# Kernel optimization log

Measured on AMD Instinct MI355X. Metric: run time of the kernel, lower is better.

Reference implementation:

```python
import jax, jax.numpy as jnp
import numpy as np

B, N, E, H = 8, 2048, 768, 8
D = E // H  # head dim = 96


def setup_inputs() -> dict:
    key = jax.random.key(0)
    ks = jax.random.split(key, 9)
    s = 0.02
    return {
        "x": jax.random.normal(ks[0], (B, N, E), dtype=jnp.float32),
        "Wq": jax.random.normal(ks[1], (E, E), dtype=jnp.float32) * s,
        "bq": jax.random.normal(ks[2], (E,), dtype=jnp.float32) * s,
        "Wk": jax.random.normal(ks[3], (E, E), dtype=jnp.float32) * s,
        "bk": jax.random.normal(ks[4], (E,), dtype=jnp.float32) * s,
        "Wv": jax.random.normal(ks[5], (E, E), dtype=jnp.float32) * s,
        "bv": jax.random.normal(ks[6], (E,), dtype=jnp.float32) * s,
        "Wo": jax.random.normal(ks[7], (E, E), dtype=jnp.float32) * s,
        "bo": jax.random.normal(ks[8], (E,), dtype=jnp.float32) * s,
    }


def _split_heads(t):
    # [b, n, (h d)] -> [b, h, n, d]
    b, n, e = t.shape
    return t.reshape(b, n, H, D).transpose(0, 2, 1, 3)


def reference(x, Wq, bq, Wk, bk, Wv, bv, Wo, bo):
    q = _split_heads(x @ Wq + bq)
    k = _split_heads(x @ Wk + bk)
    v = _split_heads(x @ Wv + bv)
    energy = jnp.einsum("bhqd,bhkd->bhqk", q, k)
    # Faithful quirk of the source: softmax first, THEN divide by sqrt(emb_size)
    att = jax.nn.softmax(energy, axis=-1) / jnp.sqrt(jnp.float32(E))
    out = jnp.einsum("bhqk,bhkd->bhqd", att, v)
    out = out.transpose(0, 2, 1, 3).reshape(x.shape[0], x.shape[1], E)
    return out @ Wo + bo
```

## Files before the change

### kernel.cpp

```cpp
#include <hip/hip_runtime.h>
#include <hip/hip_bf16.h>
#include <stdint.h>

#define BATCH 8
#define NSEQ  2048
#define EMB   768
#define NH    8
#define HD    96

typedef unsigned short u16;
typedef __attribute__((ext_vector_type(8))) short short8;
typedef __attribute__((ext_vector_type(4))) float f32x4;
typedef __attribute__((ext_vector_type(16))) float f32x16;

static __device__ __forceinline__ u16 f2bf(float f) {
  union { float f; uint32_t u; } c{f};
  uint32_t u = c.u;
  return (u16)((u + 0x7FFFu + ((u >> 16) & 1u)) >> 16);
}

__global__ __launch_bounds__(256) void k_convert_x(const float* __restrict__ x,
                                                   u16* __restrict__ xb) {
  size_t i = ((size_t)blockIdx.x * 256 + threadIdx.x) * 8;
  float4 a = *(const float4*)(x + i);
  float4 b = *(const float4*)(x + i + 4);
  short8 o;
  o[0] = f2bf(a.x); o[1] = f2bf(a.y); o[2] = f2bf(a.z); o[3] = f2bf(a.w);
  o[4] = f2bf(b.x); o[5] = f2bf(b.y); o[6] = f2bf(b.z); o[7] = f2bf(b.w);
  *(short8*)(xb + i) = o;
}

__global__ __launch_bounds__(256) void k_wtrans(const float* __restrict__ Wq,
                                                const float* __restrict__ Wk,
                                                const float* __restrict__ Wv,
                                                const float* __restrict__ Wo,
                                                u16* __restrict__ WTall) {
  int z = blockIdx.z;
  const float* W = (z == 0) ? Wq : (z == 1) ? Wk : (z == 2) ? Wv : Wo;
  u16* WT = WTall + (size_t)z * EMB * EMB;
  __shared__ float tile[32][33];
  int o0 = blockIdx.x * 32, i0 = blockIdx.y * 32;
  int tx = threadIdx.x, ty = threadIdx.y;
#pragma unroll
  for (int r = 0; r < 4; ++r)
    tile[ty * 4 + r][tx] = W[(size_t)(i0 + ty * 4 + r) * EMB + o0 + tx];
  __syncthreads();
#pragma unroll
  for (int r = 0; r < 4; ++r)
    WT[(size_t)(o0 + ty * 4 + r) * EMB + i0 + tx] = f2bf(tile[tx][ty * 4 + r]);
}

template <bool OUTF32>
static __device__ __forceinline__ void gemm_body(const u16* __restrict__ A,
                                                 const u16* __restrict__ WT,
                                                 const float* __restrict__ bias,
                                                 void* __restrict__ out,
                                                 int m0, int n0, float oscale) {
  __shared__ u16 As[128 * 64];
  __shared__ u16 Bs[128 * 64];
  const int t = threadIdx.x;
  const int w = t >> 6, l = t & 63;
  const int lr = l & 15, lg = l >> 4;
  const int wm = (w >> 1) * 64, wn = (w & 1) * 64;
  f32x4 acc[4][4] = {};
  for (int kt = 0; kt < 12; ++kt) {
    const int k0 = kt * 64;
#pragma unroll
    for (int i = 0; i < 4; ++i) {
      int g = (w * 4 + i) * 64 + l;
      int m = g >> 3, k8 = (g & 7) * 8;
      const u16* sa = A + (size_t)(m0 + m) * EMB + k0 + k8;
      __builtin_amdgcn_global_load_lds((const __attribute__((address_space(1))) void*)sa,
                                       (__attribute__((address_space(3))) void*)&As[(w * 4 + i) * 512],
                                       16, 0, 0);
      const u16* sb = WT + (size_t)(n0 + m) * EMB + k0 + k8;
      __builtin_amdgcn_global_load_lds((const __attribute__((address_space(1))) void*)sb,
                                       (__attribute__((address_space(3))) void*)&Bs[(w * 4 + i) * 512],
                                       16, 0, 0);
    }
    __syncthreads();
#pragma unroll
    for (int ks = 0; ks < 2; ++ks) {
      short8 af[4], bfr[4];
#pragma unroll
      for (int mf = 0; mf < 4; ++mf)
        af[mf] = *(const short8*)&As[(wm + mf * 16 + lr) * 64 + ks * 32 + lg * 8];
#pragma unroll
      for (int nf = 0; nf < 4; ++nf)
        bfr[nf] = *(const short8*)&Bs[(wn + nf * 16 + lr) * 64 + ks * 32 + lg * 8];
#pragma unroll
      for (int mf = 0; mf < 4; ++mf)
#pragma unroll
        for (int nf = 0; nf < 4; ++nf)
          acc[mf][nf] = __builtin_amdgcn_mfma_f32_16x16x32_bf16(af[mf], bfr[nf], acc[mf][nf], 0, 0, 0);
    }
    __syncthreads();
  }
#pragma unroll
  for (int nf = 0; nf < 4; ++nf) {
    int col = n0 + wn + nf * 16 + lr;
    float bv = bias[col];
#pragma unroll
    for (int mf = 0; mf < 4; ++mf)
#pragma unroll
      for (int r = 0; r < 4; ++r) {
        int row = m0 + wm + mf * 16 + lg * 4 + r;
        float v = (acc[mf][nf][r] + bv) * oscale;
        if (OUTF32)
          ((float*)out)[(size_t)row * EMB + col] = v;
        else
          ((u16*)out)[(size_t)row * EMB + col] = f2bf(v);
      }
  }
}

__global__ __launch_bounds__(256) void k_qkv_gemm(const u16* __restrict__ X,
                                                  const u16* __restrict__ WTall,
                                                  const float* __restrict__ bq,
                                                  const float* __restrict__ bk,
                                                  const float* __restrict__ bv,
                                                  u16* __restrict__ Q, u16* __restrict__ K,
                                                  u16* __restrict__ V) {
  int z = blockIdx.z;
  const u16* WT = WTall + (size_t)z * EMB * EMB;
  const float* bias = (z == 0) ? bq : (z == 1) ? bk : bv;
  u16* out = (z == 0) ? Q : (z == 1) ? K : V;
  float sc = (z == 0) ? 1.4426950408889634f : 1.0f;
  gemm_body<false>(X, WT, bias, out, blockIdx.x * 128, blockIdx.y * 128, sc);
}

__global__ __launch_bounds__(256) void k_out_gemm(const u16* __restrict__ AO,
                                                  const u16* __restrict__ WTo,
                                                  const float* __restrict__ bo,
                                                  float* __restrict__ out) {
  gemm_body<true>(AO, WTo, bo, out, blockIdx.x * 128, blockIdx.y * 128, 1.0f);
}

__global__ __launch_bounds__(256) void k_vtrans(const u16* __restrict__ V,
                                                u16* __restrict__ VT) {
  const int bh = blockIdx.y, b = bh >> 3, h = bh & 7;
  const int n0 = blockIdx.x * 128;
  __shared__ u16 LT[96][136];
  const int t = threadIdx.x;
#pragma unroll
  for (int i = 0; i < 6; ++i) {
    int c = i * 256 + t;
    int n = c / 12, d8 = (c % 12) * 8;
    short8 v = *(const short8*)(V + ((size_t)(b * NSEQ + n0 + n)) * EMB + h * HD + d8);
#pragma unroll
    for (int j = 0; j < 8; ++j) LT[d8 + j][n] = (u16)v[j];
  }
  __syncthreads();
#pragma unroll
  for (int i = 0; i < 6; ++i) {
    int c = i * 256 + t;
    int d = c / 16, n8 = (c % 16) * 8;
    short8 v = *(const short8*)&LT[d][n8];
    *(short8*)(VT + ((size_t)bh * HD + d) * NSEQ + n0 + n8) = v;
  }
}

static __device__ __forceinline__ void exp_sum(f32x16& s, float& ls) {
#pragma unroll
  for (int i = 0; i < 16; i += 4) {
    float e0, e1, e2, e3;
    asm("v_exp_f32 %0, %1" : "=v"(e0) : "v"(s[i + 0]));
    asm("v_exp_f32 %0, %1" : "=v"(e1) : "v"(s[i + 1]));
    asm("v_exp_f32 %0, %1" : "=v"(e2) : "v"(s[i + 2]));
    asm("v_exp_f32 %0, %1" : "=v"(e3) : "v"(s[i + 3]));
    s[i + 0] = e0; s[i + 1] = e1; s[i + 2] = e2; s[i + 3] = e3;
    ls += (e0 + e1) + (e2 + e3);
  }
}

template <int RB>
static __device__ __forceinline__ short8 pack_pa(const f32x16& s) {
  uint32_t w0, w1, w2, w3;
  asm("v_cvt_pk_bf16_f32 %0, %1, %2" : "=v"(w0) : "v"(s[RB + 0]), "v"(s[RB + 1]));
  asm("v_cvt_pk_bf16_f32 %0, %1, %2" : "=v"(w1) : "v"(s[RB + 2]), "v"(s[RB + 3]));
  asm("v_cvt_pk_bf16_f32 %0, %1, %2" : "=v"(w2) : "v"(s[RB + 4]), "v"(s[RB + 5]));
  asm("v_cvt_pk_bf16_f32 %0, %1, %2" : "=v"(w3) : "v"(s[RB + 6]), "v"(s[RB + 7]));
  asm("v_permlane32_swap_b32 %0, %1" : "+v"(w0), "+v"(w2));
  asm("v_permlane32_swap_b32 %0, %1" : "+v"(w1), "+v"(w3));
  union { uint32_t u[4]; short8 s8; } pu;
  pu.u[0] = w0; pu.u[1] = w1; pu.u[2] = w2; pu.u[3] = w3;
  return pu.s8;
}

__global__ __launch_bounds__(256, 2) void k_attn(const u16* __restrict__ Q,
                                                 const u16* __restrict__ K,
                                                 const u16* __restrict__ VT,
                                                 u16* __restrict__ AO) {
  __shared__ u16 Ks[2][64][104];
  __shared__ u16 Vs[2][96][72];
  const int t = threadIdx.x, w = t >> 6, l = t & 63;
  const int l31 = l & 31, hi = l >> 5;
  const int bh = blockIdx.y, b = bh >> 3, h = bh & 7;
  const int q0 = blockIdx.x * 256 + w * 64;
  const size_t rowBase = (size_t)b * NSEQ;

  short8 qf0[6], qf1[6];
#pragma unroll
  for (int ksd = 0; ksd < 6; ++ksd) {
    qf0[ksd] = *(const short8*)(Q + (rowBase + q0 + l31) * EMB + h * HD + ksd * 16 + hi * 8);
    qf1[ksd] = *(const short8*)(Q + (rowBase + q0 + 32 + l31) * EMB + h * HD + ksd * 16 + hi * 8);
  }

  f32x16 oacc0[3] = {}, oacc1[3] = {};
  float ls0 = 0.f, ls1 = 0.f;

  short8 kr[3], vr[3];
  auto load_tile = [&](int kv0) {
#pragma unroll
    for (int i = 0; i < 3; ++i) {
      int c = i * 256 + t;
      int kn = c / 12, kd8 = (c % 12) * 8;
      kr[i] = *(const short8*)(K + (rowBase + kv0 + kn) * EMB + h * HD + kd8);
      int vd = c / 8, vn8 = (c % 8) * 8;
      vr[i] = *(const short8*)(VT + ((size_t)bh * HD + vd) * NSEQ + kv0 + vn8);
    }
  };
  auto write_tile = [&](int buf) {
#pragma unroll
    for (int i = 0; i < 3; ++i) {
      int c = i * 256 + t;
      int kn = c / 12, kd8 = (c % 12) * 8;
      *(short8*)&Ks[buf][kn][kd8] = kr[i];
      int vd = c / 8, vn8 = (c % 8) * 8;
      *(short8*)&Vs[buf][vd][vn8] = vr[i];
    }
  };

  load_tile(0);
  write_tile(0);
  load_tile(64);
  __syncthreads();

  for (int tt = 0; tt < 32; ++tt) {
    const int cur = tt & 1;
    if (tt < 31) write_tile(cur ^ 1);
    if (tt < 30) load_tile((tt + 2) * 64);

    f32x16 s00 = {}, s01 = {};
    __builtin_amdgcn_s_setprio(1);
#pragma unroll
    for (int ksd = 0; ksd < 6; ++ksd) {
      short8 kf = *(const short8*)&Ks[cur][l31][ksd * 16 + hi * 8];
      s00 = __builtin_amdgcn_mfma_f32_32x32x16_bf16(kf, qf0[ksd], s00, 0, 0, 0);
      s01 = __builtin_amdgcn_mfma_f32_32x32x16_bf16(kf, qf1[ksd], s01, 0, 0, 0);
    }
    __builtin_amdgcn_s_setprio(0);
    exp_sum(s00, ls0);
    exp_sum(s01, ls1);
    short8 paA00 = pack_pa<0>(s00), paA01 = pack_pa<8>(s00);
    short8 paA10 = pack_pa<0>(s01), paA11 = pack_pa<8>(s01);
    __builtin_amdgcn_s_setprio(1);
#pragma unroll
    for (int dt = 0; dt < 3; ++dt) {
      short8 vfa = *(const short8*)&Vs[cur][dt * 32 + l31][hi * 8];
      short8 vfb = *(const short8*)&Vs[cur][dt * 32 + l31][16 + hi * 8];
      oacc0[dt] = __builtin_amdgcn_mfma_f32_32x32x16_bf16(paA00, vfa, oacc0[dt], 0, 0, 0);
      oacc1[dt] = __builtin_amdgcn_mfma_f32_32x32x16_bf16(paA10, vfa, oacc1[dt], 0, 0, 0);
      oacc0[dt] = __builtin_amdgcn_mfma_f32_32x32x16_bf16(paA01, vfb, oacc0[dt], 0, 0, 0);
      oacc1[dt] = __builtin_amdgcn_mfma_f32_32x32x16_bf16(paA11, vfb, oacc1[dt], 0, 0, 0);
    }
    __builtin_amdgcn_s_setprio(0);

    f32x16 s10 = {}, s11 = {};
    __builtin_amdgcn_s_setprio(1);
#pragma unroll
    for (int ksd = 0; ksd < 6; ++ksd) {
      short8 kf = *(const short8*)&Ks[cur][32 + l31][ksd * 16 + hi * 8];
      s10 = __builtin_amdgcn_mfma_f32_32x32x16_bf16(kf, qf0[ksd], s10, 0, 0, 0);
      s11 = __builtin_amdgcn_mfma_f32_32x32x16_bf16(kf, qf1[ksd], s11, 0, 0, 0);
    }
    __builtin_amdgcn_s_setprio(0);
    exp_sum(s10, ls0);
    exp_sum(s11, ls1);
    short8 paB00 = pack_pa<0>(s10), paB01 = pack_pa<8>(s10);
    short8 paB10 = pack_pa<0>(s11), paB11 = pack_pa<8>(s11);
    __builtin_amdgcn_s_setprio(1);
#pragma unroll
    for (int dt = 0; dt < 3; ++dt) {
      short8 vfa = *(const short8*)&Vs[cur][dt * 32 + l31][32 + hi * 8];
      short8 vfb = *(const short8*)&Vs[cur][dt * 32 + l31][48 + hi * 8];
      oacc0[dt] = __builtin_amdgcn_mfma_f32_32x32x16_bf16(paB00, vfa, oacc0[dt], 0, 0, 0);
      oacc1[dt] = __builtin_amdgcn_mfma_f32_32x32x16_bf16(paB10, vfa, oacc1[dt], 0, 0, 0);
      oacc0[dt] = __builtin_amdgcn_mfma_f32_32x32x16_bf16(paB01, vfb, oacc0[dt], 0, 0, 0);
      oacc1[dt] = __builtin_amdgcn_mfma_f32_32x32x16_bf16(paB11, vfb, oacc1[dt], 0, 0, 0);
    }
    __builtin_amdgcn_s_setprio(0);

    __syncthreads();
  }

  ls0 += __shfl_xor(ls0, 32, 64);
  ls1 += __shfl_xor(ls1, 32, 64);
  float inv0 = 1.0f / (ls0 * 27.712812921102035f);
  float inv1 = 1.0f / (ls1 * 27.712812921102035f);
#pragma unroll
  for (int r = 0; r < 16; ++r) {
    int qreg = (r & 3) + 8 * (r >> 2) + 4 * hi;
    float iq0 = __shfl(inv0, qreg, 64);
    float iq1 = __shfl(inv1, qreg, 64);
#pragma unroll
    for (int dt = 0; dt < 3; ++dt) {
      AO[(rowBase + q0 + qreg) * EMB + h * HD + dt * 32 + l31] = f2bf(oacc0[dt][r] * iq0);
      AO[(rowBase + q0 + 32 + qreg) * EMB + h * HD + dt * 32 + l31] = f2bf(oacc1[dt][r] * iq1);
    }
  }
}

extern "C" void kernel_launch(void* const* d_in, const int* in_sizes, int n_in,
                              void* d_out, int out_size, void* d_ws, size_t ws_size,
                              hipStream_t stream) {
  (void)in_sizes; (void)n_in; (void)out_size; (void)ws_size;
  const float* x  = (const float*)d_in[0];
  const float* Wq = (const float*)d_in[1];
  const float* bq = (const float*)d_in[2];
  const float* Wk = (const float*)d_in[3];
  const float* bk = (const float*)d_in[4];
  const float* Wv = (const float*)d_in[5];
  const float* bv = (const float*)d_in[6];
  const float* Wo = (const float*)d_in[7];
  const float* bo = (const float*)d_in[8];
  float* out = (float*)d_out;

  char* ws = (char*)d_ws;
  const size_t SZ = (size_t)BATCH * NSEQ * EMB * 2;
  u16* XB = (u16*)(ws);
  u16* QB = (u16*)(ws + SZ);
  u16* KB = (u16*)(ws + 2 * SZ);
  u16* VB = (u16*)(ws + 3 * SZ);
  u16* WT = (u16*)(ws + 4 * SZ);
  u16* VT = XB;
  u16* AO = VB;

  k_convert_x<<<dim3(6144), dim3(256), 0, stream>>>(x, XB);
  k_wtrans<<<dim3(24, 24, 4), dim3(32, 8), 0, stream>>>(Wq, Wk, Wv, Wo, WT);
  k_qkv_gemm<<<dim3(128, 6, 3), dim3(256), 0, stream>>>(XB, WT, bq, bk, bv, QB, KB, VB);
  k_vtrans<<<dim3(16, 64), dim3(256), 0, stream>>>(VB, VT);
  k_attn<<<dim3(8, 64), dim3(256), 0, stream>>>(QB, KB, VT, AO);
  k_out_gemm<<<dim3(128, 6), dim3(256), 0, stream>>>(AO, WT + (size_t)3 * EMB * EMB, bo, out);
}
```

Before: 274.2 us.

## Rewrite projection GEMMs as 256x256 double-buffered pipelined tiles with swizzled LDS

Replaces the 128x128 single-buffered GEMM used for the QKV and output projections with a 256x256 tile, 512-thread kernel. It double-buffers LDS, interleaves global-to-LDS prefetch of the next K tiles between MFMA quadrants, and uses s_setprio and sched barriers. An XOR swizzle is added to avoid LDS bank conflicts. The aim is to hide load latency and raise data reuse per block, at the cost of far fewer blocks (576 for QKV, 192 for the output GEMM), which may underfill the GPU, plus 128KB of LDS per block.

```diff
diff --git a/kernel.cpp b/kernel.cpp
--- a/kernel.cpp
+++ b/kernel.cpp
@@ -50,61 +50,147 @@
     WT[(size_t)(o0 + ty * 4 + r) * EMB + i0 + tx] = f2bf(tile[tx][ty * 4 + r]);
 }
 
+
+#define SBAR() do { __builtin_amdgcn_sched_barrier(0); __builtin_amdgcn_s_barrier(); } while (0)
+
+#define MMA_QUAD(MFH, NFH, BF)                                                        \
+  do {                                                                                \
+    __builtin_amdgcn_s_setprio(1);                                                    \
+    _Pragma("unroll") for (int mf2 = 0; mf2 < 4; ++mf2)                               \
+      _Pragma("unroll") for (int nf2 = 0; nf2 < 2; ++nf2)                             \
+        _Pragma("unroll") for (int ks = 0; ks < 2; ++ks)                              \
+          acc[(MFH) * 4 + mf2][(NFH) * 2 + nf2] =                                     \
+              __builtin_amdgcn_mfma_f32_16x16x32_bf16(                                \
+                  af[mf2][ks], BF[nf2][ks],                                           \
+                  acc[(MFH) * 4 + mf2][(NFH) * 2 + nf2], 0, 0, 0);                    \
+    __builtin_amdgcn_s_setprio(0);                                                    \
+  } while (0)
+
 template <bool OUTF32>
-static __device__ __forceinline__ void gemm_body(const u16* __restrict__ A,
-                                                 const u16* __restrict__ WT,
-                                                 const float* __restrict__ bias,
-                                                 void* __restrict__ out,
-                                                 int m0, int n0, float oscale) {
-  __shared__ u16 As[128 * 64];
-  __shared__ u16 Bs[128 * 64];
+static __device__ __forceinline__ void gemm256_body(const u16* __restrict__ Aop,
+                                                    const u16* __restrict__ WT,
+                                                    const float* __restrict__ bias,
+                                                    void* __restrict__ out,
+                                                    int m0, int n0, float oscale) {
+  __shared__ u16 As[2][256 * 64];
+  __shared__ u16 Bs[2][256 * 64];
   const int t = threadIdx.x;
   const int w = t >> 6, l = t & 63;
   const int lr = l & 15, lg = l >> 4;
-  const int wm = (w >> 1) * 64, wn = (w & 1) * 64;
-  f32x4 acc[4][4] = {};
-  for (int kt = 0; kt < 12; ++kt) {
-    const int k0 = kt * 64;
-#pragma unroll
-    for (int i = 0; i < 4; ++i) {
-      int g = (w * 4 + i) * 64 + l;
-      int m = g >> 3, k8 = (g & 7) * 8;
-      const u16* sa = A + (size_t)(m0 + m) * EMB + k0 + k8;
-      __builtin_amdgcn_global_load_lds((const __attribute__((address_space(1))) void*)sa,
-                                       (__attribute__((address_space(3))) void*)&As[(w * 4 + i) * 512],
-                                       16, 0, 0);
-      const u16* sb = WT + (size_t)(n0 + m) * EMB + k0 + k8;
-      __builtin_amdgcn_global_load_lds((const __attribute__((address_space(1))) void*)sb,
-                                       (__attribute__((address_space(3))) void*)&Bs[(w * 4 + i) * 512],
-                                       16, 0, 0);
-    }
-    __syncthreads();
-#pragma unroll
-    for (int ks = 0; ks < 2; ++ks) {
-      short8 af[4], bfr[4];
-#pragma unroll
-      for (int mf = 0; mf < 4; ++mf)
-        af[mf] = *(const short8*)&As[(wm + mf * 16 + lr) * 64 + ks * 32 + lg * 8];
-#pragma unroll
-      for (int nf = 0; nf < 4; ++nf)
-        bfr[nf] = *(const short8*)&Bs[(wn + nf * 16 + lr) * 64 + ks * 32 + lg * 8];
-#pragma unroll
-      for (int mf = 0; mf < 4; ++mf)
-#pragma unroll
-        for (int nf = 0; nf < 4; ++nf)
-          acc[mf][nf] = __builtin_amdgcn_mfma_f32_16x16x32_bf16(af[mf], bfr[nf], acc[mf][nf], 0, 0, 0);
-    }
-    __syncthreads();
-  }
+  const int wr = w >> 2, wc = w & 3;
+  const u16* PA = Aop + (size_t)m0 * EMB;
+  const u16* PB = WT + (size_t)n0 * EMB;
+
+  f32x4 acc[8][4] = {};
+  short8 af[4][2], bfA[2][2], bfB[2][2];
+
+  auto stage = [&](const u16* P, u16* lds, int kt, int i) {
+    int gb = i * 512 + w * 64;
+    int g = gb + l;
+    int row = g >> 3;
+    int cb = ((g & 7) * 16) ^ ((row & 7) << 4);
+    const u16* src = P + (size_t)row * EMB + kt * 64 + (cb >> 1);
+    __builtin_amdgcn_global_load_lds((const __attribute__((address_space(1))) void*)src,
+                                     (__attribute__((address_space(3))) void*)(lds + gb * 8),
+                                     16, 0, 0);
+  };
+  auto rdA = [&](const u16* lds, int mfh) {
+#pragma unroll
+    for (int mf2 = 0; mf2 < 4; ++mf2)
+#pragma unroll
+      for (int ks = 0; ks < 2; ++ks) {
+        int row = wr * 128 + (mfh * 4 + mf2) * 16 + lr;
+        int cb = (ks * 64 + lg * 16) ^ ((lr & 7) << 4);
+        af[mf2][ks] = *(const short8*)(lds + row * 64 + (cb >> 1));
+      }
+  };
+  auto rdB = [&](const u16* lds, int nfh, short8 (&bf)[2][2]) {
+#pragma unroll
+    for (int nf2 = 0; nf2 < 2; ++nf2)
+#pragma unroll
+      for (int ks = 0; ks < 2; ++ks) {
+        int row = wc * 64 + (nfh * 2 + nf2) * 16 + lr;
+        int cb = (ks * 64 + lg * 16) ^ ((lr & 7) << 4);
+        bf[nf2][ks] = *(const short8*)(lds + row * 64 + (cb >> 1));
+      }
+  };
+
+#pragma unroll
+  for (int i = 0; i < 4; ++i) stage(PA, As[0], 0, i);
+#pragma unroll
+  for (int i = 0; i < 4; ++i) stage(PB, Bs[0], 0, i);
+#pragma unroll
+  for (int i = 0; i < 4; ++i) stage(PA, As[1], 1, i);
+#pragma unroll
+  for (int i = 0; i < 4; ++i) stage(PB, Bs[1], 1, i);
+  asm volatile("s_waitcnt vmcnt(8)" ::: "memory");
+  __builtin_amdgcn_s_barrier();
+
+  for (int it = 0; it < 6; ++it) {
+    const int kt0 = 2 * it;
+    const bool nl = (it < 5);
+    rdA(As[0], 0);
+    rdB(Bs[0], 0, bfA);
+    SBAR();
+    MMA_QUAD(0, 0, bfA);
+    SBAR();
+    rdB(Bs[0], 1, bfB);
+    SBAR();
+    MMA_QUAD(0, 1, bfB);
+    SBAR();
+    rdA(As[0], 1);
+    if (nl) { stage(PB, Bs[0], kt0 + 2, 0); stage(PB, Bs[0], kt0 + 2, 1); }
+    SBAR();
+    MMA_QUAD(1, 1, bfB);
+    SBAR();
+    if (nl) {
+      stage(PB, Bs[0], kt0 + 2, 2); stage(PB, Bs[0], kt0 + 2, 3);
+#pragma unroll
+      for (int i = 0; i < 4; ++i) stage(PA, As[0], kt0 + 2, i);
+    }
+    SBAR();
+    MMA_QUAD(1, 0, bfA);
+    __builtin_amdgcn_sched_barrier(0);
+    if (nl) asm volatile("s_waitcnt vmcnt(8)" ::: "memory");
+    else    asm volatile("s_waitcnt vmcnt(0)" ::: "memory");
+    __builtin_amdgcn_s_barrier();
+
+    rdA(As[1], 0);
+    rdB(Bs[1], 0, bfA);
+    SBAR();
+    MMA_QUAD(0, 0, bfA);
+    SBAR();
+    rdB(Bs[1], 1, bfB);
+    SBAR();
+    MMA_QUAD(0, 1, bfB);
+    SBAR();
+    rdA(As[1], 1);
+    if (nl) { stage(PB, Bs[1], kt0 + 3, 0); stage(PB, Bs[1], kt0 + 3, 1); }
+    SBAR();
+    MMA_QUAD(1, 1, bfB);
+    SBAR();
+    if (nl) {
+      stage(PB, Bs[1], kt0 + 3, 2); stage(PB, Bs[1], kt0 + 3, 3);
+#pragma unroll
+      for (int i = 0; i < 4; ++i) stage(PA, As[1], kt0 + 3, i);
+    }
+    SBAR();
+    MMA_QUAD(1, 0, bfA);
+    __builtin_amdgcn_sched_barrier(0);
+    if (nl) asm volatile("s_waitcnt vmcnt(8)" ::: "memory");
+    else    asm volatile("s_waitcnt vmcnt(0)" ::: "memory");
+    __builtin_amdgcn_s_barrier();
+  }
+
 #pragma unroll
   for (int nf = 0; nf < 4; ++nf) {
-    int col = n0 + wn + nf * 16 + lr;
+    int col = n0 + wc * 64 + nf * 16 + lr;
     float bv = bias[col];
 #pragma unroll
-    for (int mf = 0; mf < 4; ++mf)
+    for (int mf = 0; mf < 8; ++mf)
 #pragma unroll
       for (int r = 0; r < 4; ++r) {
-        int row = m0 + wm + mf * 16 + lg * 4 + r;
+        int row = m0 + wr * 128 + mf * 16 + lg * 4 + r;
         float v = (acc[mf][nf][r] + bv) * oscale;
         if (OUTF32)
           ((float*)out)[(size_t)row * EMB + col] = v;
@@ -114,26 +200,26 @@
   }
 }
 
-__global__ __launch_bounds__(256) void k_qkv_gemm(const u16* __restrict__ X,
-                                                  const u16* __restrict__ WTall,
-                                                  const float* __restrict__ bq,
-                                                  const float* __restrict__ bk,
-                                                  const float* __restrict__ bv,
-                                                  u16* __restrict__ Q, u16* __restrict__ K,
-                                                  u16* __restrict__ V) {
+__global__ __launch_bounds__(512, 2) void k_qkv_gemm(const u16* __restrict__ X,
+                                                     const u16* __restrict__ WTall,
+                                                     const float* __restrict__ bq,
+                                                     const float* __restrict__ bk,
+                                                     const float* __restrict__ bv,
+                                                     u16* __restrict__ Q, u16* __restrict__ K,
+                                                     u16* __restrict__ V) {
   int z = blockIdx.z;
   const u16* WT = WTall + (size_t)z * EMB * EMB;
   const float* bias = (z == 0) ? bq : (z == 1) ? bk : bv;
   u16* out = (z == 0) ? Q : (z == 1) ? K : V;
   float sc = (z == 0) ? 1.4426950408889634f : 1.0f;
-  gemm_body<false>(X, WT, bias, out, blockIdx.x * 128, blockIdx.y * 128, sc);
-}
-
-__global__ __launch_bounds__(256) void k_out_gemm(const u16* __restrict__ AO,
-                                                  const u16* __restrict__ WTo,
-                                                  const float* __restrict__ bo,
-                                                  float* __restrict__ out) {
-  gemm_body<true>(AO, WTo, bo, out, blockIdx.x * 128, blockIdx.y * 128, 1.0f);
+  gemm256_body<false>(X, WT, bias, out, blockIdx.x * 256, blockIdx.y * 256, sc);
+}
+
+__global__ __launch_bounds__(512, 2) void k_out_gemm(const u16* __restrict__ AO,
+                                                     const u16* __restrict__ WTo,
+                                                     const float* __restrict__ bo,
+                                                     float* __restrict__ out) {
+  gemm256_body<true>(AO, WTo, bo, out, blockIdx.x * 256, blockIdx.y * 256, 1.0f);
 }
 
 __global__ __launch_bounds__(256) void k_vtrans(const u16* __restrict__ V,
@@ -338,8 +424,8 @@
 
   k_convert_x<<<dim3(6144), dim3(256), 0, stream>>>(x, XB);
   k_wtrans<<<dim3(24, 24, 4), dim3(32, 8), 0, stream>>>(Wq, Wk, Wv, Wo, WT);
-  k_qkv_gemm<<<dim3(128, 6, 3), dim3(256), 0, stream>>>(XB, WT, bq, bk, bv, QB, KB, VB);
+  k_qkv_gemm<<<dim3(64, 3, 3), dim3(512), 0, stream>>>(XB, WT, bq, bk, bv, QB, KB, VB);
   k_vtrans<<<dim3(16, 64), dim3(256), 0, stream>>>(VB, VT);
   k_attn<<<dim3(8, 64), dim3(256), 0, stream>>>(QB, KB, VT, AO);
-  k_out_gemm<<<dim3(128, 6), dim3(256), 0, stream>>>(AO, WT + (size_t)3 * EMB * EMB, bo, out);
-}
+  k_out_gemm<<<dim3(64, 3), dim3(512), 0, stream>>>(AO, WT + (size_t)3 * EMB * EMB, bo, out);
+}
```

Result: faster. 246.1 us (-10.2%).
